# Optimization experiments

Hardware: AMD Instinct MI355X
Metric: run time of the kernel (lower is better)

## Reference

```python
import jax, jax.numpy as jnp
import numpy as np


def setup_inputs() -> dict:
    key = jax.random.key(0)
    k1, k2 = jax.random.split(key)
    B, L = 128, 1024
    inp = jax.random.normal(k1, (B, L), dtype=jnp.float32)
    target = jax.random.randint(k2, (B, L), 0, 2).astype(jnp.int64)
    return {"input": inp, "target": target}


def reference(input, target):
    # y_i[b,i]: label i is positive; y_bar[b,j]: label j is negative
    y = target == 1
    # truth[b,i,j] = y[b,i] & ~y[b,j]
    truth = y[:, :, None] & (~y)[:, None, :]
    # exp_m[b,i,j] = exp(input[b,j] - input[b,i])
    exp_m = jnp.exp(input[:, None, :] - input[:, :, None])
    length = truth.sum(axis=(1, 2)).astype(input.dtype)  # [B]
    inner = jnp.where(truth, exp_m, jnp.zeros((), input.dtype)).sum(axis=(1, 2))  # [B]
    losses = inner / length
    return losses.sum()
```

## Files before the change

kernel.cpp:

```cpp
#include <hip/hip_runtime.h>
#include <hip/hip_bf16.h>


#define B_DIM 128
#define L_DIM 1024

__global__ void bpmll_zero_out(float* out) { out[0] = 0.0f; }

__global__ __launch_bounds__(256) void bpmll_kernel(const float* __restrict__ inp,
                                                    const int* __restrict__ tgt,
                                                    float* __restrict__ out) {
    const int b = blockIdx.x;
    const int t = threadIdx.x;

    const float4* in4 = (const float4*)(inp + (size_t)b * L_DIM);
    const int4*   tg4 = (const int4*)(tgt + (size_t)b * L_DIM);

    float4 x = in4[t];
    int4   y = tg4[t];

    float s_neg = 0.0f;
    float s_pos = 0.0f;
    int   npos  = 0;

    if (y.x == 1) { s_pos += __expf(-x.x) * 0.0f + expf(-x.x); npos++; } else { s_neg += expf(x.x); }
    if (y.y == 1) { s_pos += expf(-x.y); npos++; } else { s_neg += expf(x.y); }
    if (y.z == 1) { s_pos += expf(-x.z); npos++; } else { s_neg += expf(x.z); }
    if (y.w == 1) { s_pos += expf(-x.w); npos++; } else { s_neg += expf(x.w); }

    #pragma unroll
    for (int off = 32; off > 0; off >>= 1) {
        s_neg += __shfl_down(s_neg, off);
        s_pos += __shfl_down(s_pos, off);
        npos  += __shfl_down(npos,  off);
    }

    __shared__ float sh_neg[4], sh_pos[4];
    __shared__ int   sh_np[4];
    const int wave = t >> 6;
    if ((t & 63) == 0) {
        sh_neg[wave] = s_neg;
        sh_pos[wave] = s_pos;
        sh_np[wave]  = npos;
    }
    __syncthreads();

    if (t == 0) {
        float tn = sh_neg[0] + sh_neg[1] + sh_neg[2] + sh_neg[3];
        float tp = sh_pos[0] + sh_pos[1] + sh_pos[2] + sh_pos[3];
        int   np = sh_np[0] + sh_np[1] + sh_np[2] + sh_np[3];
        int   nn = L_DIM - np;
        float len = (float)np * (float)nn;
        float loss = (len > 0.0f) ? (tn * tp) / len : 0.0f;
        atomicAdd(out, loss);
    }
}

extern "C" void kernel_launch(void* const* d_in, const int* in_sizes, int n_in,
                              void* d_out, int out_size, void* d_ws, size_t ws_size,
                              hipStream_t stream) {
    const float* inp = (const float*)d_in[0];
    const int*   tgt = (const int*)d_in[1];
    float* out = (float*)d_out;

    bpmll_zero_out<<<1, 1, 0, stream>>>(out);
    bpmll_kernel<<<B_DIM, 256, 0, stream>>>(inp, tgt, out);
}
```

Before: 57.34 us.

## Fuse zero-init and reduction into a single-block kernel without atomics

```diff
diff --git a/kernel.cpp b/kernel.cpp
--- a/kernel.cpp
+++ b/kernel.cpp
@@ -2,57 +2,86 @@
 #include <hip/hip_bf16.h>
 
 
-#define B_DIM 128
 #define L_DIM 1024
+#define ROWS_PER_WAVE 8
 
-__global__ void bpmll_zero_out(float* out) { out[0] = 0.0f; }
+__global__ __launch_bounds__(1024) void bpmll_single(const float* __restrict__ inp,
+                                                     const int* __restrict__ tgt,
+                                                     float* __restrict__ out) {
+    const int t    = threadIdx.x;
+    const int wave = t >> 6;
+    const int lane = t & 63;
 
-__global__ __launch_bounds__(256) void bpmll_kernel(const float* __restrict__ inp,
-                                                    const int* __restrict__ tgt,
-                                                    float* __restrict__ out) {
-    const int b = blockIdx.x;
-    const int t = threadIdx.x;
-
-    const float4* in4 = (const float4*)(inp + (size_t)b * L_DIM);
-    const int4*   tg4 = (const int4*)(tgt + (size_t)b * L_DIM);
-
-    float4 x = in4[t];
-    int4   y = tg4[t];
-
-    float s_neg = 0.0f;
-    float s_pos = 0.0f;
-    int   npos  = 0;
-
-    if (y.x == 1) { s_pos += __expf(-x.x) * 0.0f + expf(-x.x); npos++; } else { s_neg += expf(x.x); }
-    if (y.y == 1) { s_pos += expf(-x.y); npos++; } else { s_neg += expf(x.y); }
-    if (y.z == 1) { s_pos += expf(-x.z); npos++; } else { s_neg += expf(x.z); }
-    if (y.w == 1) { s_pos += expf(-x.w); npos++; } else { s_neg += expf(x.w); }
+    float acc = 0.0f;
 
     #pragma unroll
-    for (int off = 32; off > 0; off >>= 1) {
-        s_neg += __shfl_down(s_neg, off);
-        s_pos += __shfl_down(s_pos, off);
-        npos  += __shfl_down(npos,  off);
+    for (int r = 0; r < ROWS_PER_WAVE; ++r) {
+        const int row = wave * ROWS_PER_WAVE + r;
+        const float4* in4 = (const float4*)(inp + (size_t)row * L_DIM);
+        const int4*   tg4 = (const int4*)(tgt + (size_t)row * L_DIM);
+
+        float s_neg = 0.0f;
+        float s_pos = 0.0f;
+        int   np    = 0;
+
+        #pragma unroll
+        for (int it = 0; it < L_DIM / (64 * 4); ++it) {
+            float4 x = in4[it * 64 + lane];
+            int4   y = tg4[it * 64 + lane];
+
+            {
+                bool p = (y.x == 1);
+                float e = __expf(p ? -x.x : x.x);
+                s_pos += p ? e : 0.0f;
+                s_neg += p ? 0.0f : e;
+                np    += p ? 1 : 0;
+            }
+            {
+                bool p = (y.y == 1);
+                float e = __expf(p ? -x.y : x.y);
+                s_pos += p ? e : 0.0f;
+                s_neg += p ? 0.0f : e;
+                np    += p ? 1 : 0;
+            }
+            {
+                bool p = (y.z == 1);
+                float e = __expf(p ? -x.z : x.z);
+                s_pos += p ? e : 0.0f;
+                s_neg += p ? 0.0f : e;
+                np    += p ? 1 : 0;
+            }
+            {
+                bool p = (y.w == 1);
+                float e = __expf(p ? -x.w : x.w);
+                s_pos += p ? e : 0.0f;
+                s_neg += p ? 0.0f : e;
+                np    += p ? 1 : 0;
+            }
+        }
+
+        #pragma unroll
+        for (int off = 32; off > 0; off >>= 1) {
+            s_neg += __shfl_down(s_neg, off);
+            s_pos += __shfl_down(s_pos, off);
+            np    += __shfl_down(np,    off);
+        }
+
+        if (lane == 0) {
+            int nn = L_DIM - np;
+            float len = (float)np * (float)nn;
+            acc += (len > 0.0f) ? (s_neg * s_pos) / len : 0.0f;
+        }
     }
 
-    __shared__ float sh_neg[4], sh_pos[4];
-    __shared__ int   sh_np[4];
-    const int wave = t >> 6;
-    if ((t & 63) == 0) {
-        sh_neg[wave] = s_neg;
-        sh_pos[wave] = s_pos;
-        sh_np[wave]  = npos;
-    }
+    __shared__ float sh[16];
+    if (lane == 0) sh[wave] = acc;
     __syncthreads();
 
     if (t == 0) {
-        float tn = sh_neg[0] + sh_neg[1] + sh_neg[2] + sh_neg[3];
-        float tp = sh_pos[0] + sh_pos[1] + sh_pos[2] + sh_pos[3];
-        int   np = sh_np[0] + sh_np[1] + sh_np[2] + sh_np[3];
-        int   nn = L_DIM - np;
-        float len = (float)np * (float)nn;
-        float loss = (len > 0.0f) ? (tn * tp) / len : 0.0f;
-        atomicAdd(out, loss);
+        float s = 0.0f;
+        #pragma unroll
+        for (int i = 0; i < 16; ++i) s += sh[i];
+        out[0] = s;
     }
 }
 
@@ -63,6 +92,5 @@
     const int*   tgt = (const int*)d_in[1];
     float* out = (float*)d_out;
 
-    bpmll_zero_out<<<1, 1, 0, stream>>>(out);
-    bpmll_kernel<<<B_DIM, 256, 0, stream>>>(inp, tgt, out);
+    bpmll_single<<<1, 1024, 0, stream>>>(inp, tgt, out);
 }
```

Result: slower. 65.78 us (+14.7%).
